# Kernel tuning notes

Measured on AMD Instinct MI355X. Metric: run time of the kernel, lower is better.

## Reference

```python
import jax, jax.numpy as jnp
import numpy as np

B, T, D_IN = 32, 32, 128
N_SLOTS, M_LEN = 512, 64
NUM_SHIFT, NUM_READ, NUM_WRITE = 3, 4, 1
CTRL_DIM = 256
READ_HEAD_LEN = 3 + M_LEN + NUM_SHIFT            # k, beta, g, s, gamma
WRITE_HEAD_LEN = READ_HEAD_LEN + 2 * M_LEN       # + erase, add vectors
INSTR_DIM = NUM_READ * READ_HEAD_LEN + NUM_WRITE * WRITE_HEAD_LEN


def setup_inputs() -> dict:
    key = jax.random.key(0)
    ks = jax.random.split(key, 4)
    def glorot(k, shape):
        lim = np.sqrt(6.0 / (shape[0] + shape[1])).astype(np.float32)
        return jax.random.uniform(k, shape, jnp.float32, -lim, lim)
    return {
        "x": jax.random.normal(ks[0], (B, T, D_IN), jnp.float32),
        "Wc": glorot(ks[1], (D_IN + NUM_READ * M_LEN, CTRL_DIM)),
        "bc": jnp.zeros((CTRL_DIM,), jnp.float32),
        "heads_kernel": glorot(ks[2], (CTRL_DIM, INSTR_DIM)),
        "heads_bias": jnp.zeros((INSTR_DIM,), jnp.float32),
    }


def _parse_heads(h):
    # h: (B, H, 3 + M + S) -> k, beta, g, s, gamma per _get_weight_vector
    k = h[..., :M_LEN]
    b = jnp.exp(h[..., M_LEN])
    g = jax.nn.sigmoid(h[..., M_LEN + 1])
    s = jax.nn.softmax(h[..., M_LEN + 2:M_LEN + 2 + NUM_SHIFT], axis=-1)
    t = jax.nn.softplus(h[..., M_LEN + 2 + NUM_SHIFT]) + 1.0
    return k, b, g, s, t


def _address(Mem, w_prev, k, b, g, s, t):
    # Mem:(B,N,M) k:(B,H,M) w_prev:(B,H,N) b,g,t:(B,H) s:(B,H,S)
    eps = 1e-8
    Mn = jnp.linalg.norm(Mem, axis=-1)                       # (B,N)
    kn = jnp.linalg.norm(k, axis=-1)                         # (B,H)
    sim = jnp.einsum('bhm,bnm->bhn', k, Mem) / (kn[..., None] * Mn[:, None, :] + eps)
    wc = jax.nn.softmax(b[..., None] * sim, axis=-1)         # content
    wg = g[..., None] * wc + (1.0 - g[..., None]) * w_prev   # gate
    half = NUM_SHIFT // 2                                    # circular shift conv
    wsh = sum(s[..., i:i + 1] * jnp.roll(wg, i - half, axis=-1) for i in range(NUM_SHIFT))
    wt = wsh ** t[..., None]                                 # sharpen
    return wt / (jnp.sum(wt, axis=-1, keepdims=True) + eps)


def _ntm_forward(x, Wc, bc, heads_kernel, heads_bias):
    def step(carry, x_t):
        r, rw, ww, Mem = carry
        # dense controller on [x_t, old read vectors]
        ctrl_in = jnp.concatenate([x_t, r.reshape(B, -1)], axis=-1)
        h = jnp.tanh(ctrl_in @ Wc + bc)                      # controller_out == instr
        instr = h @ heads_kernel + heads_bias                # (B, INSTR_DIM)
        rh = instr[:, :NUM_READ * READ_HEAD_LEN].reshape(B, NUM_READ, READ_HEAD_LEN)
        wh = instr[:, NUM_READ * READ_HEAD_LEN:].reshape(B, NUM_WRITE, WRITE_HEAD_LEN)
        rw_n = _address(Mem, rw, *_parse_heads(rh))
        ww_n = _address(Mem, ww, *_parse_heads(wh[..., :READ_HEAD_LEN]))
        e = wh[..., READ_HEAD_LEN:READ_HEAD_LEN + M_LEN]     # raw erase (no sigmoid, as in source)
        a = wh[..., READ_HEAD_LEN + M_LEN:]                  # raw add
        # erase all heads, then add all heads (source loops erase first)
        Mem = Mem * jnp.prod(1.0 - ww_n[..., :, None] * e[..., None, :], axis=1)
        Mem = Mem + jnp.einsum('bwn,bwm->bnm', ww_n, a)
        r_n = jnp.einsum('bnm,brn->brm', Mem, rw_n)          # read
        return (r_n, rw_n, ww_n, Mem), h

    init = (jnp.zeros((B, NUM_READ, M_LEN), jnp.float32),
            jnp.zeros((B, NUM_READ, N_SLOTS), jnp.float32),
            jnp.zeros((B, NUM_WRITE, N_SLOTS), jnp.float32),
            jnp.zeros((B, N_SLOTS, M_LEN), jnp.float32))
    _, outs = jax.lax.scan(step, init, jnp.swapaxes(x, 0, 1))  # time-major
    return outs[-1]  # return_sequences=False -> last controller output (B, CTRL_DIM)


def reference(x, Wc, bc, heads_kernel, heads_bias):
    return _ntm_forward(x, Wc, bc, heads_kernel, heads_bias)
```

## Files before the change

### kernel.cpp

```cpp
#include <hip/hip_runtime.h>
#include <math.h>

#define BB 32
#define TT 32
#define D_INX 128
#define NSLOT 512
#define MLEN 64
#define NREAD 4
#define NHEAD 5
#define CDIM 256
#define IDIM 478
#define RHL 70
#define NT 512

#define XP_SZ   1048576
#define WCT_OFF XP_SZ
#define HKB_OFF (XP_SZ + 262144)

typedef short bf8 __attribute__((ext_vector_type(8)));
typedef float f32x4 __attribute__((ext_vector_type(4)));

struct SMem {
    float mem[NSLOT * MLEN];
    float w4[NSLOT * 4];
    float ww[NSLOT];
    float mn[NSLOT];
    float ctrl[256];
    float h[CDIM];
    float instr[480];
    float k[NHEAD * MLEN];
    float e[MLEN];
    float a[MLEN];
    float u[NHEAD * NSLOT];
};

__device__ __forceinline__ float rlane(float v, int l) {
    return __int_as_float(__builtin_amdgcn_readlane(__float_as_int(v), l));
}

__device__ __forceinline__ void cvt_hi_lo(const float* a, bf8* hi, bf8* lo) {
    union { unsigned u[4]; bf8 v; } H, L;
#pragma unroll
    for (int p = 0; p < 4; ++p) {
        unsigned hu;
        asm("v_cvt_pk_bf16_f32 %0, %1, %2" : "=v"(hu) : "v"(a[2 * p]), "v"(a[2 * p + 1]));
        H.u[p] = hu;
        float h0 = __uint_as_float(hu << 16);
        float h1 = __uint_as_float(hu & 0xffff0000u);
        float l0 = a[2 * p] - h0;
        float l1 = a[2 * p + 1] - h1;
        unsigned lu;
        asm("v_cvt_pk_bf16_f32 %0, %1, %2" : "=v"(lu) : "v"(l0), "v"(l1));
        L.u[p] = lu;
    }
    *hi = H.v; *lo = L.v;
}

__global__ void pack_kernel(const float* __restrict__ Wc, const float* __restrict__ Hk,
                            float* __restrict__ wct, float* __restrict__ hkb)
{
    int idx = blockIdx.x * 256 + threadIdx.x;
    if (idx < 256 * 256) {
        int i = idx >> 8, col = idx & 255;
        wct[((i >> 3) * 256 + col) * 8 + (i & 7)] = Wc[(128 + i) * 256 + col];
    }
    if (idx < 256 * 478) {
        int i = idx / 478, col = idx - i * 478;
        hkb[((i >> 3) * 478 + col) * 8 + (i & 7)] = Hk[i * 478 + col];
    }
}

__global__ __launch_bounds__(256)
void xpart_kernel(const float* __restrict__ x, const float* __restrict__ Wc,
                  const float* __restrict__ bc, float* __restrict__ xp)
{
    __shared__ float xs[D_INX];
    const int bt = blockIdx.x, col = threadIdx.x;
    if (col < D_INX) xs[col] = x[(size_t)bt * D_INX + col];
    __syncthreads();
    float acc = bc[col];
#pragma unroll 8
    for (int k = 0; k < D_INX; ++k) acc += xs[k] * Wc[k * 256 + col];
    xp[(size_t)bt * CDIM + col] = acc;
}

#define P1_CHUNK(cg_) do {                                                      \
    const float4 w0 = wqa[(cg_) * 512];                                         \
    const float4 w1 = wqa[(cg_) * 512 + 1];                                     \
    const int k0 = (cg_) * 8;                                                   \
    float a0 = rlane(creg[(k0 + 0) >> 6], (k0 + 0) & 63);                       \
    float a1 = rlane(creg[(k0 + 1) >> 6], (k0 + 1) & 63);                       \
    float a2 = rlane(creg[(k0 + 2) >> 6], (k0 + 2) & 63);                       \
    float a3 = rlane(creg[(k0 + 3) >> 6], (k0 + 3) & 63);                       \
    float a4 = rlane(creg[(k0 + 4) >> 6], (k0 + 4) & 63);                       \
    float a5 = rlane(creg[(k0 + 5) >> 6], (k0 + 5) & 63);                       \
    float a6 = rlane(creg[(k0 + 6) >> 6], (k0 + 6) & 63);                       \
    float a7 = rlane(creg[(k0 + 7) >> 6], (k0 + 7) & 63);                       \
    accs[(cg_) & 3] += w0.x * a0 + w0.y * a1 + w0.z * a2 + w0.w * a3            \
                     + w1.x * a4 + w1.y * a5 + w1.z * a6 + w1.w * a7;           \
} while (0)

__global__ __launch_bounds__(NT, 2)
void ntm_kernel(const float* __restrict__ xp,
                const float* __restrict__ hb,
                const float* __restrict__ wct,
                const float* __restrict__ hkb,
                float* __restrict__ out)
{
    extern __shared__ float smem_f[];
    SMem* sc = (SMem*)smem_f;

    const int b    = blockIdx.x;
    const int tid  = threadIdx.x;
    const int lane = tid & 63;
    const int wave = tid >> 6;

    const int col   = tid & 255;
    const int halfw = tid >> 8;

    const float hbv = (tid < IDIM) ? hb[tid] : 0.f;

    {
        float4 z4 = make_float4(0.f, 0.f, 0.f, 0.f);
        float4* m4 = (float4*)sc->mem;
        for (int i = tid; i < NSLOT * MLEN / 4; i += NT) m4[i] = z4;
        for (int i = tid; i < NSLOT * 4; i += NT) sc->w4[i] = 0.f;
        if (tid < NSLOT) sc->ww[tid] = 0.f;
        if (tid < 256) sc->ctrl[tid] = 0.f;
        for (int i = tid; i < 2048; i += NT) sc->u[i] = 0.f;
    }
    __syncthreads();

    for (int t = 0; t < TT; ++t) {
        if (tid < 256) {
            float s = sc->u[tid];
#pragma unroll
            for (int w = 1; w < 8; ++w) s += sc->u[w * 256 + tid];
            sc->ctrl[tid] = s;
        }
        __syncthreads();

        {
            const float xpv = xp[(size_t)(b * TT + t) * CDIM + col];

            float creg[4];
            creg[0] = sc->ctrl[lane];
            creg[1] = sc->ctrl[64 + lane];
            creg[2] = sc->ctrl[128 + lane];
            creg[3] = sc->ctrl[192 + lane];

            const float4* wqa = (const float4*)wct + col * 2;
            float accs[4] = {0.f, 0.f, 0.f, 0.f};
            if (halfw == 0) {
#pragma unroll
                for (int cc = 0; cc < 16; ++cc) P1_CHUNK(cc);
            } else {
#pragma unroll
                for (int cc = 0; cc < 16; ++cc) P1_CHUNK(16 + cc);
            }
            float s = (accs[0] + accs[1]) + (accs[2] + accs[3]);
            if (halfw == 1) sc->u[col] = s;
            __syncthreads();
            if (halfw == 0) {
                float z = xpv + s + sc->u[col];
                z = fminf(fmaxf(z, -15.f), 15.f);
                float ex = __expf(2.f * z);
                float hv = (ex - 1.f) / (ex + 1.f);
                sc->h[col] = hv;
                if (t == TT - 1) out[(size_t)b * CDIM + col] = hv;
            }
        }
        if (t == TT - 1) break;
        __syncthreads();

        {
            float hreg[4];
#pragma unroll
            for (int j = 0; j < 4; ++j) hreg[j] = sc->h[64 * j + lane];
            if (tid < IDIM) {
                const float4* wq2a = (const float4*)hkb + tid * 2;
                float accs[4] = {0.f, 0.f, 0.f, 0.f};
#pragma unroll
                for (int c = 0; c < 32; ++c) {
                    const float4 w0 = wq2a[c * 956];
                    const float4 w1 = wq2a[c * 956 + 1];
                    const int k0 = c * 8;
                    float a0 = rlane(hreg[(k0 + 0) >> 6], (k0 + 0) & 63);
                    float a1 = rlane(hreg[(k0 + 1) >> 6], (k0 + 1) & 63);
                    float a2 = rlane(hreg[(k0 + 2) >> 6], (k0 + 2) & 63);
                    float a3 = rlane(hreg[(k0 + 3) >> 6], (k0 + 3) & 63);
                    float a4 = rlane(hreg[(k0 + 4) >> 6], (k0 + 4) & 63);
                    float a5 = rlane(hreg[(k0 + 5) >> 6], (k0 + 5) & 63);
                    float a6 = rlane(hreg[(k0 + 6) >> 6], (k0 + 6) & 63);
                    float a7 = rlane(hreg[(k0 + 7) >> 6], (k0 + 7) & 63);
                    accs[c & 3] += w0.x * a0 + w0.y * a1 + w0.z * a2 + w0.w * a3
                                 + w1.x * a4 + w1.y * a5 + w1.z * a6 + w1.w * a7;
                }
                float acc = hbv + (accs[0] + accs[1]) + (accs[2] + accs[3]);
                sc->instr[tid] = acc;
                if (tid < 350) {
                    int hh = (tid * 937) >> 16;
                    int m = tid - hh * RHL;
                    if (m < MLEN) sc->k[hh * MLEN + m] = acc;
                } else if (tid < 414) {
                    sc->e[tid - 350] = acc;
                } else {
                    sc->a[tid - 414] = acc;
                }
            }
        }
        __syncthreads();

        {
            const int q   = lane >> 4;
            const int r15 = lane & 15;

            bf8 bhi[2], blo[2];
#pragma unroll
            for (int kc = 0; kc < 2; ++kc) {
                float kb[8];
                if (r15 < NHEAD) {
                    const float4* k4 = (const float4*)(sc->k + r15 * MLEN + kc * 32 + q * 8);
                    float4 kv0 = k4[0], kv1 = k4[1];
                    kb[0] = kv0.x; kb[1] = kv0.y; kb[2] = kv0.z; kb[3] = kv0.w;
                    kb[4] = kv1.x; kb[5] = kv1.y; kb[6] = kv1.z; kb[7] = kv1.w;
                } else {
#pragma unroll
                    for (int i = 0; i < 8; ++i) kb[i] = 0.f;
                }
                cvt_hi_lo(kb, &bhi[kc], &blo[kc]);
            }

#pragma unroll
            for (int tt2 = 0; tt2 < 4; ++tt2) {
                const int tbase = wave * 64 + tt2 * 16;
                const int n = tbase + r15;
                const int nx = n & 15;
                const float4* m4 = (const float4*)sc->mem + n * 16;
                f32x4 acc = {0.f, 0.f, 0.f, 0.f};
                float nsq = 0.f;
#pragma unroll
                for (int kc = 0; kc < 2; ++kc) {
                    const int j0 = kc * 8 + q * 2;
                    float4 av0 = m4[j0 ^ nx];
                    float4 av1 = m4[(j0 + 1) ^ nx];
                    float aa[8];
                    aa[0] = av0.x; aa[1] = av0.y; aa[2] = av0.z; aa[3] = av0.w;
                    aa[4] = av1.x; aa[5] = av1.y; aa[6] = av1.z; aa[7] = av1.w;
#pragma unroll
                    for (int i = 0; i < 8; ++i) nsq += aa[i] * aa[i];
                    bf8 ahi, alo;
                    cvt_hi_lo(aa, &ahi, &alo);
                    acc = __builtin_amdgcn_mfma_f32_16x16x32_bf16(ahi, bhi[kc], acc, 0, 0, 0);
                    acc = __builtin_amdgcn_mfma_f32_16x16x32_bf16(ahi, blo[kc], acc, 0, 0, 0);
                    acc = __builtin_amdgcn_mfma_f32_16x16x32_bf16(alo, bhi[kc], acc, 0, 0, 0);
                }
                nsq += __shfl_xor(nsq, 16);
                nsq += __shfl_xor(nsq, 32);
                if (q == 0) sc->mn[n] = sqrtf(nsq);
                if (r15 < NHEAD) {
                    float4 st;
                    st.x = acc[0]; st.y = acc[1]; st.z = acc[2]; st.w = acc[3];
                    *(float4*)&sc->u[r15 * NSLOT + tbase + q * 4] = st;
                }
            }
        }
        __syncthreads();

        if (wave < NHEAD) {
            const int h = wave;
            const float* ins = sc->instr + h * RHL;
            float kv = ins[lane];
            float sq = kv * kv;
#pragma unroll
            for (int off = 32; off; off >>= 1) sq += __shfl_xor(sq, off);
            float kn = sqrtf(sq);
            float beta = __expf(ins[64]);
            float g = 1.f / (1.f + __expf(-ins[65]));
            float v0 = ins[66], v1 = ins[67], v2 = ins[68];
            float mx3 = fmaxf(v0, fmaxf(v1, v2));
            float e0 = __expf(v0 - mx3), e1 = __expf(v1 - mx3), e2 = __expf(v2 - mx3);
            float inv3 = 1.f / (e0 + e1 + e2);
            float s0 = e0 * inv3, s1 = e1 * inv3, s2 = e2 * inv3;
            float tv = ins[69];
            float tp = fmaxf(tv, 0.f) + log1pf(__expf(-fabsf(tv))) + 1.f;

            float uu[8];
#pragma unroll
            for (int j = 0; j < 8; ++j) {
                int slot = j * 64 + lane;
                float d = sc->u[h * NSLOT + slot];
                uu[j] = beta * d / (kn * sc->mn[slot] + 1e-8f);
            }
            float m = uu[0];
#pragma unroll
            for (int j = 1; j < 8; ++j) m = fmaxf(m, uu[j]);
#pragma unroll
            for (int off = 32; off; off >>= 1) m = fmaxf(m, __shfl_xor(m, off));
            float ev[8]; float Z = 0.f;
#pragma unroll
            for (int j = 0; j < 8; ++j) { ev[j] = __expf(uu[j] - m); Z += ev[j]; }
#pragma unroll
            for (int off = 32; off; off >>= 1) Z += __shfl_xor(Z, off);
            float invZ = 1.f / Z;
            float wg[8];
#pragma unroll
            for (int j = 0; j < 8; ++j) {
                int slot = j * 64 + lane;
                float oldw = (h < 4) ? sc->w4[slot * 4 + h] : sc->ww[slot];
                wg[j] = g * ev[j] * invZ + (1.f - g) * oldw;
            }
            int lm = (lane + 63) & 63, lp = (lane + 1) & 63;
            float rm[8], rp[8];
#pragma unroll
            for (int j = 0; j < 8; ++j) {
                float sm = (lane == 63) ? wg[(j + 7) & 7] : wg[j];
                float sp = (lane == 0)  ? wg[(j + 1) & 7] : wg[j];
                rm[j] = __shfl(sm, lm);
                rp[j] = __shfl(sp, lp);
            }
            float wt[8]; float S = 0.f;
#pragma unroll
            for (int j = 0; j < 8; ++j) {
                float wsh = s0 * rp[j] + s1 * wg[j] + s2 * rm[j];
                wt[j] = __builtin_amdgcn_exp2f(tp * __builtin_amdgcn_logf(wsh));
                S += wt[j];
            }
#pragma unroll
            for (int off = 32; off; off >>= 1) S += __shfl_xor(S, off);
            float invS = 1.f / (S + 1e-8f);
#pragma unroll
            for (int j = 0; j < 8; ++j) {
                int slot = j * 64 + lane;
                float wnew = wt[j] * invS;
                if (h < 4) sc->w4[slot * 4 + h] = wnew;
                else       sc->ww[slot] = wnew;
            }
        }
        __syncthreads();

        {
            const int rg = lane >> 4, j = lane & 15, base = wave * 64;
            const float4 ev = ((const float4*)sc->e)[j];
            const float4 av = ((const float4*)sc->a)[j];
            float4* m4 = (float4*)sc->mem;
#pragma unroll
            for (int i = 0; i < 16; ++i) {
                const int n = base + 4 * i + rg;
                const int idx = n * 16 + (j ^ (n & 15));
                float4 mv = m4[idx];
                const float wv = sc->ww[n];
                mv.x = mv.x * (1.f - wv * ev.x) + wv * av.x;
                mv.y = mv.y * (1.f - wv * ev.y) + wv * av.y;
                mv.z = mv.z * (1.f - wv * ev.z) + wv * av.z;
                mv.w = mv.w * (1.f - wv * ev.w) + wv * av.w;
                m4[idx] = mv;
            }
            const int q = rg, r15 = j;
            bf8 ahi[2], alo[2];
#pragma unroll
            for (int kc = 0; kc < 2; ++kc) {
                float ab[8];
#pragma unroll
                for (int i = 0; i < 8; ++i) {
                    const int n2 = base + kc * 32 + q * 8 + i;
                    ab[i] = (r15 < 4) ? sc->w4[n2 * 4 + r15] : 0.f;
                }
                cvt_hi_lo(ab, &ahi[kc], &alo[kc]);
            }
#pragma unroll
            for (int tt2 = 0; tt2 < 4; ++tt2) {
                f32x4 acc = {0.f, 0.f, 0.f, 0.f};
#pragma unroll
                for (int kc = 0; kc < 2; ++kc) {
                    float bb[8];
#pragma unroll
                    for (int i = 0; i < 8; ++i) {
                        const int n2 = base + kc * 32 + q * 8 + i;
                        const int cc = tt2 * 16 + r15;
                        bb[i] = sc->mem[n2 * 64 + (((cc >> 2) ^ (n2 & 15)) << 2) + (cc & 3)];
                    }
                    bf8 bhi, blo;
                    cvt_hi_lo(bb, &bhi, &blo);
                    acc = __builtin_amdgcn_mfma_f32_16x16x32_bf16(ahi[kc], bhi, acc, 0, 0, 0);
                    acc = __builtin_amdgcn_mfma_f32_16x16x32_bf16(ahi[kc], blo, acc, 0, 0, 0);
                    acc = __builtin_amdgcn_mfma_f32_16x16x32_bf16(alo[kc], bhi, acc, 0, 0, 0);
                }
                if (q == 0) {
#pragma unroll
                    for (int reg = 0; reg < 4; ++reg)
                        sc->u[wave * 256 + reg * 64 + tt2 * 16 + r15] = acc[reg];
                }
            }
        }
        __syncthreads();
    }
}

extern "C" void kernel_launch(void* const* d_in, const int* in_sizes, int n_in,
                              void* d_out, int out_size, void* d_ws, size_t ws_size,
                              hipStream_t stream) {
    const float* x  = (const float*)d_in[0];
    const float* Wc = (const float*)d_in[1];
    const float* bc = (const float*)d_in[2];
    const float* Hk = (const float*)d_in[3];
    const float* hb = (const float*)d_in[4];
    float* out = (float*)d_out;

    float* xp  = (float*)d_ws;
    float* wct = (float*)((char*)d_ws + WCT_OFF);
    float* hkb = (float*)((char*)d_ws + HKB_OFF);

    static_assert(sizeof(SMem) <= 163840, "LDS overflow");
    (void)hipFuncSetAttribute((const void*)ntm_kernel,
                              hipFuncAttributeMaxDynamicSharedMemorySize,
                              (int)sizeof(SMem));

    hipLaunchKernelGGL(pack_kernel, dim3(478), dim3(256), 0, stream, Wc, Hk, wct, hkb);
    hipLaunchKernelGGL(xpart_kernel, dim3(BB * TT), dim3(256), 0, stream, x, Wc, bc, xp);
    hipLaunchKernelGGL(ntm_kernel, dim3(BB), dim3(NT), sizeof(SMem), stream,
                       xp, hb, wct, hkb, out);
}
```

Measured before the change: 742.7 us.

## Fold controller partial-sum reduction into matvec and prefetch memory tiles early

Removes the separate ctrl reduction pass and its barrier: each thread half now sums the eight partial buffers for its own columns directly into registers, and the cross-half exchange moves to a separate u region. It also hoists the first half of the memory-row loads, norm partials and bf16 hi/lo splitting into the heads matvec phase, so that work overlaps before the barrier and the similarity MFMA phase does less. The cost is more live registers, which may hurt occupancy or cause spills. It also assumes the u buffer is large enough for the 2048+256 offset.

```diff
diff --git a/kernel.cpp b/kernel.cpp
--- a/kernel.cpp
+++ b/kernel.cpp
@@ -126,28 +126,27 @@
         for (int i = tid; i < NSLOT * MLEN / 4; i += NT) m4[i] = z4;
         for (int i = tid; i < NSLOT * 4; i += NT) sc->w4[i] = 0.f;
         if (tid < NSLOT) sc->ww[tid] = 0.f;
-        if (tid < 256) sc->ctrl[tid] = 0.f;
         for (int i = tid; i < 2048; i += NT) sc->u[i] = 0.f;
     }
     __syncthreads();
 
     for (int t = 0; t < TT; ++t) {
-        if (tid < 256) {
-            float s = sc->u[tid];
-#pragma unroll
-            for (int w = 1; w < 8; ++w) s += sc->u[w * 256 + tid];
-            sc->ctrl[tid] = s;
-        }
-        __syncthreads();
-
         {
             const float xpv = xp[(size_t)(b * TT + t) * CDIM + col];
 
             float creg[4];
-            creg[0] = sc->ctrl[lane];
-            creg[1] = sc->ctrl[64 + lane];
-            creg[2] = sc->ctrl[128 + lane];
-            creg[3] = sc->ctrl[192 + lane];
+            {
+                const int jb = halfw * 2;
+                float s0a = sc->u[jb * 64 + lane];
+                float s1a = sc->u[(jb + 1) * 64 + lane];
+#pragma unroll
+                for (int w = 1; w < 8; ++w) {
+                    s0a += sc->u[w * 256 + jb * 64 + lane];
+                    s1a += sc->u[w * 256 + (jb + 1) * 64 + lane];
+                }
+                creg[jb] = s0a; creg[jb + 1] = s1a;
+                creg[jb ^ 2] = 0.f; creg[(jb ^ 2) + 1] = 0.f;
+            }
 
             const float4* wqa = (const float4*)wct + col * 2;
             float accs[4] = {0.f, 0.f, 0.f, 0.f};
@@ -159,10 +158,10 @@
                 for (int cc = 0; cc < 16; ++cc) P1_CHUNK(16 + cc);
             }
             float s = (accs[0] + accs[1]) + (accs[2] + accs[3]);
-            if (halfw == 1) sc->u[col] = s;
+            if (halfw == 1) sc->u[2048 + col] = s;
             __syncthreads();
             if (halfw == 0) {
-                float z = xpv + s + sc->u[col];
+                float z = xpv + s + sc->u[2048 + col];
                 z = fminf(fmaxf(z, -15.f), 15.f);
                 float ex = __expf(2.f * z);
                 float hv = (ex - 1.f) / (ex + 1.f);
@@ -173,6 +172,8 @@
         if (t == TT - 1) break;
         __syncthreads();
 
+        bf8 pahi[4], palo[4];
+        float pnsq[4];
         {
             float hreg[4];
 #pragma unroll
@@ -208,6 +209,26 @@
                     sc->a[tid - 414] = acc;
                 }
             }
+            {
+                const int q = lane >> 4, r15 = lane & 15;
+#pragma unroll
+                for (int tt2 = 0; tt2 < 4; ++tt2) {
+                    const int n = wave * 64 + tt2 * 16 + r15;
+                    const int nx = n & 15;
+                    const float4* m4p = (const float4*)sc->mem + n * 16;
+                    const int j0 = q * 2;
+                    float4 av0 = m4p[j0 ^ nx];
+                    float4 av1 = m4p[(j0 + 1) ^ nx];
+                    float aa[8];
+                    aa[0] = av0.x; aa[1] = av0.y; aa[2] = av0.z; aa[3] = av0.w;
+                    aa[4] = av1.x; aa[5] = av1.y; aa[6] = av1.z; aa[7] = av1.w;
+                    float ns = 0.f;
+#pragma unroll
+                    for (int i = 0; i < 8; ++i) ns += aa[i] * aa[i];
+                    pnsq[tt2] = ns;
+                    cvt_hi_lo(aa, &pahi[tt2], &palo[tt2]);
+                }
+            }
         }
         __syncthreads();
 
@@ -238,23 +259,23 @@
                 const int nx = n & 15;
                 const float4* m4 = (const float4*)sc->mem + n * 16;
                 f32x4 acc = {0.f, 0.f, 0.f, 0.f};
-                float nsq = 0.f;
-#pragma unroll
-                for (int kc = 0; kc < 2; ++kc) {
-                    const int j0 = kc * 8 + q * 2;
-                    float4 av0 = m4[j0 ^ nx];
-                    float4 av1 = m4[(j0 + 1) ^ nx];
-                    float aa[8];
-                    aa[0] = av0.x; aa[1] = av0.y; aa[2] = av0.z; aa[3] = av0.w;
-                    aa[4] = av1.x; aa[5] = av1.y; aa[6] = av1.z; aa[7] = av1.w;
-#pragma unroll
-                    for (int i = 0; i < 8; ++i) nsq += aa[i] * aa[i];
-                    bf8 ahi, alo;
-                    cvt_hi_lo(aa, &ahi, &alo);
-                    acc = __builtin_amdgcn_mfma_f32_16x16x32_bf16(ahi, bhi[kc], acc, 0, 0, 0);
-                    acc = __builtin_amdgcn_mfma_f32_16x16x32_bf16(ahi, blo[kc], acc, 0, 0, 0);
-                    acc = __builtin_amdgcn_mfma_f32_16x16x32_bf16(alo, bhi[kc], acc, 0, 0, 0);
-                }
+                acc = __builtin_amdgcn_mfma_f32_16x16x32_bf16(pahi[tt2], bhi[0], acc, 0, 0, 0);
+                acc = __builtin_amdgcn_mfma_f32_16x16x32_bf16(pahi[tt2], blo[0], acc, 0, 0, 0);
+                acc = __builtin_amdgcn_mfma_f32_16x16x32_bf16(palo[tt2], bhi[0], acc, 0, 0, 0);
+                const int j0 = 8 + q * 2;
+                float4 av0 = m4[j0 ^ nx];
+                float4 av1 = m4[(j0 + 1) ^ nx];
+                float aa[8];
+                aa[0] = av0.x; aa[1] = av0.y; aa[2] = av0.z; aa[3] = av0.w;
+                aa[4] = av1.x; aa[5] = av1.y; aa[6] = av1.z; aa[7] = av1.w;
+                float nsq = pnsq[tt2];
+#pragma unroll
+                for (int i = 0; i < 8; ++i) nsq += aa[i] * aa[i];
+                bf8 ahi, alo;
+                cvt_hi_lo(aa, &ahi, &alo);
+                acc = __builtin_amdgcn_mfma_f32_16x16x32_bf16(ahi, bhi[1], acc, 0, 0, 0);
+                acc = __builtin_amdgcn_mfma_f32_16x16x32_bf16(ahi, blo[1], acc, 0, 0, 0);
+                acc = __builtin_amdgcn_mfma_f32_16x16x32_bf16(alo, bhi[1], acc, 0, 0, 0);
                 nsq += __shfl_xor(nsq, 16);
                 nsq += __shfl_xor(nsq, 32);
                 if (q == 0) sc->mn[n] = sqrtf(nsq);
```

Result: slower. 827.7 us (+11.5%).
